# Optimization experiments

Measured on AMD Instinct MI355X. Metric: run time of the kernel, lower is better.

## Reference

```python
import jax, jax.numpy as jnp
import numpy as np

LN_EPS = 1e-5

def _layernorm(x):
    # LayerNorm over last dim, no affine params (elementwise_affine=False)
    mu = jnp.mean(x, axis=-1, keepdims=True)
    var = jnp.var(x, axis=-1, keepdims=True)
    return (x - mu) / jnp.sqrt(var + LN_EPS)

def setup_inputs() -> dict:
    key = jax.random.key(0)
    k1, k2 = jax.random.split(key)
    B, S, D_IN, D_OUT = 4, 2048, 4096, 4096
    x = jax.random.normal(k1, (B, S, D_IN), dtype=jnp.float32)
    # kaiming-uniform-ish init scale (exact distribution irrelevant for correctness baseline)
    bound = 1.0 / np.sqrt(D_IN)
    weight = jax.random.uniform(k2, (D_OUT, D_IN), dtype=jnp.float32, minval=-bound, maxval=bound)
    return {"x": x, "weight": weight}

def reference(x, weight):
    # weight mean-centering and scalar scale beta
    w_centered = weight - jnp.mean(weight)
    beta = jnp.mean(jnp.abs(w_centered))
    x_norm = _layernorm(x)
    w_bin = jnp.sign(w_centered)                       # [D_out, D_in] in {-1,0,+1}
    out = jnp.einsum('bsi,oi->bso', x_norm, w_bin)     # dense GEMM on binarized weights
    return out * beta
```

## Files before the change

kernel.cpp:

```cpp
#include <hip/hip_runtime.h>
#include <hip/hip_bf16.h>
#include <stdint.h>


typedef __bf16 bf16x8 __attribute__((ext_vector_type(8)));
typedef float f32x4 __attribute__((ext_vector_type(4)));

#define LDS_BUF 65536


__device__ __forceinline__ void gl_lds16(const void* g, void* l) {
  __builtin_amdgcn_global_load_lds(
      (const __attribute__((address_space(1))) void*)g,
      (__attribute__((address_space(3))) void*)l,
      16, 0, 0);
}

__device__ __forceinline__ unsigned short f2bf_rne(float f) {
  unsigned int u = __float_as_uint(f);
  unsigned int r = (u + 0x7FFFu + ((u >> 16) & 1u)) >> 16;
  return (unsigned short)r;
}

__device__ __forceinline__ float wave_red(float v) {
#pragma unroll
  for (int o = 32; o > 0; o >>= 1) v += __shfl_down(v, o, 64);
  return v;
}

__device__ __forceinline__ float block_red(float v) {
  __shared__ float tmp[4];
  const int wave = threadIdx.x >> 6, lane = threadIdx.x & 63;
  v = wave_red(v);
  if (lane == 0) tmp[wave] = v;
  __syncthreads();
  float r = 0.f;
  if (threadIdx.x == 0) r = tmp[0] + tmp[1] + tmp[2] + tmp[3];
  return r;
}


__global__ void zero_kernel(float* p) {
  if (threadIdx.x < 8) p[threadIdx.x] = 0.f;
}

__global__ __launch_bounds__(256) void wsum_kernel(const float* __restrict__ w,
                                                   float* __restrict__ scal, int n4) {
  int idx = blockIdx.x * 256 + threadIdx.x;
  int stride = gridDim.x * 256;
  const float4* w4 = (const float4*)w;
  float s = 0.f;
  for (int i = idx; i < n4; i += stride) {
    float4 a = w4[i];
    s += a.x + a.y + a.z + a.w;
  }
  float tot = block_red(s);
  if (threadIdx.x == 0) atomicAdd(&scal[0], tot);
}

__global__ __launch_bounds__(256) void wbin_kernel(const float* __restrict__ w,
                                                   float* __restrict__ scal,
                                                   unsigned short* __restrict__ wb,
                                                   int n4, float inv_n) {
  const float mean = scal[0] * inv_n;
  int idx = blockIdx.x * 256 + threadIdx.x;
  int stride = gridDim.x * 256;
  const float4* w4 = (const float4*)w;
  ushort4* wb4 = (ushort4*)wb;
  float sa = 0.f;
  for (int i = idx; i < n4; i += stride) {
    float4 a = w4[i];
    float dx = a.x - mean, dy = a.y - mean, dz = a.z - mean, dw = a.w - mean;
    sa += fabsf(dx) + fabsf(dy) + fabsf(dz) + fabsf(dw);
    ushort4 o;
    o.x = dx > 0.f ? 0x3F80u : (dx < 0.f ? 0xBF80u : 0u);
    o.y = dy > 0.f ? 0x3F80u : (dy < 0.f ? 0xBF80u : 0u);
    o.z = dz > 0.f ? 0x3F80u : (dz < 0.f ? 0xBF80u : 0u);
    o.w = dw > 0.f ? 0x3F80u : (dw < 0.f ? 0xBF80u : 0u);
    wb4[i] = o;
  }
  float tot = block_red(sa);
  if (threadIdx.x == 0) atomicAdd(&scal[1], tot);
}

__global__ __launch_bounds__(256) void ln_kernel(const float* __restrict__ x,
                                                 __bf16* __restrict__ xn) {
  const int row = blockIdx.x;
  const float4* xr = (const float4*)(x + (size_t)row * 4096);
  const int tid = threadIdx.x;
  float4 v[4];
  float s = 0.f, ss = 0.f;
#pragma unroll
  for (int t = 0; t < 4; t++) {
    float4 a = xr[t * 256 + tid];
    v[t] = a;
    s += a.x + a.y + a.z + a.w;
    ss += a.x * a.x + a.y * a.y + a.z * a.z + a.w * a.w;
  }
#pragma unroll
  for (int o = 32; o > 0; o >>= 1) {
    s += __shfl_down(s, o, 64);
    ss += __shfl_down(ss, o, 64);
  }
  __shared__ float rs[8];
  const int wave = tid >> 6, lane = tid & 63;
  if (lane == 0) { rs[wave] = s; rs[4 + wave] = ss; }
  __syncthreads();
  s = rs[0] + rs[1] + rs[2] + rs[3];
  ss = rs[4] + rs[5] + rs[6] + rs[7];
  const float mu = s * (1.0f / 4096.0f);
  const float var = ss * (1.0f / 4096.0f) - mu * mu;
  const float rstd = rsqrtf(var + 1e-5f);
  ushort4* xw = (ushort4*)((unsigned short*)xn + (size_t)row * 4096);
#pragma unroll
  for (int t = 0; t < 4; t++) {
    float4 a = v[t];
    ushort4 o;
    o.x = f2bf_rne((a.x - mu) * rstd);
    o.y = f2bf_rne((a.y - mu) * rstd);
    o.z = f2bf_rne((a.z - mu) * rstd);
    o.w = f2bf_rne((a.w - mu) * rstd);
    xw[t * 256 + tid] = o;
  }
}


__global__ __launch_bounds__(512, 2) void gemm_kernel(
    const __bf16* __restrict__ A, const __bf16* __restrict__ Bm,
    float* __restrict__ C, const float* __restrict__ scal,
    float beta_scale, int M, int N, int K) {
  extern __shared__ __align__(16) char sm[];

  const int tid = threadIdx.x;
  const int wave = tid >> 6, lane = tid & 63;
  const int wm = wave >> 2, wn = wave & 3;
  const int fr = lane & 15, hi4 = lane >> 4;

  const int nwg = gridDim.x;
  const int swz = (blockIdx.x & 7) * (nwg >> 3) + (blockIdx.x >> 3);
  const int TM = M >> 8;
  const int tm = swz % TM, tn = swz / TM;
  const int rowBase = tm << 8, colBase = tn << 8;

  const int s = (tid & 7) ^ ((tid >> 3) & 7);
  const int rb = ((tid >> 2) & ~1) | (s >> 2);
  const int colOff = (s & 3) << 3;
  const __bf16* srcA0 = A + (size_t)(rowBase + (rb & 63) + ((rb >> 6) << 7)) * K + colOff;
  const __bf16* srcB0 = Bm + (size_t)(colBase + rb) * K + colOff;
  const int waveOff = wave << 10;

  int abase = (wm << 12) + (fr << 6) + (hi4 << 4);
  abase ^= ((abase >> 7) & 7) << 4;
  int bbase = ((wn >> 1) << 13) + ((wn & 1) << 12) + (fr << 6) + (hi4 << 4);
  bbase ^= ((bbase >> 7) & 7) << 4;

  char* const buf0 = sm;
  char* const buf1 = sm + LDS_BUF;

  auto stA = [&](char* buf, int k, int qm, int kt) {
    gl_lds16(srcA0 + (size_t)(qm << 6) * K + (kt + (k << 5)),
             buf + (k << 14) + (qm << 13) + waveOff);
  };
  auto stB = [&](char* buf, int k, int half, int kt) {
    gl_lds16(srcB0 + (size_t)(half << 7) * K + (kt + (k << 5)),
             buf + 32768 + (k << 14) + (half << 13) + waveOff);
  };

  f32x4 acc[8][4];
#pragma unroll
  for (int i = 0; i < 8; i++)
#pragma unroll
    for (int j = 0; j < 4; j++) acc[i][j] = (f32x4){0.f, 0.f, 0.f, 0.f};

  const int NT = K >> 6;

  stA(buf0, 0, 0, 0); stA(buf0, 0, 1, 0); stB(buf0, 0, 0, 0); stB(buf0, 0, 1, 0);
  stA(buf0, 1, 0, 0); stA(buf0, 1, 1, 0); stB(buf0, 1, 0, 0); stB(buf0, 1, 1, 0);
  stA(buf1, 0, 0, 64); stA(buf1, 0, 1, 64); stB(buf1, 0, 0, 64);
  stA(buf1, 1, 0, 64); stB(buf1, 0, 1, 64);
  asm volatile("s_waitcnt vmcnt(5)" ::: "memory");
  asm volatile("s_barrier" ::: "memory");

  for (int T = 0; T < NT; ++T) {
    char* const bc = (T & 1) ? buf1 : buf0;
    char* const bo = (T & 1) ? buf0 : buf1;
    const int kt1 = ((T + 1 < NT) ? T + 1 : NT - 1) << 6;
    const int kt2 = ((T + 2 < NT) ? T + 2 : NT - 1) << 6;

    bf16x8 a0[4], a1[4], b0[4], b1[4];

#pragma unroll
    for (int i = 0; i < 4; i++) a0[i] = *(const bf16x8*)(bc + abase + (i << 10));
#pragma unroll
    for (int j = 0; j < 4; j++) b0[j] = *(const bf16x8*)(bc + 32768 + bbase + (j << 10));
    stA(bo, 1, 1, kt1); stB(bo, 1, 0, kt1); stB(bo, 1, 1, kt1);
    asm volatile("s_barrier" ::: "memory");
    asm volatile("s_waitcnt lgkmcnt(0)" ::: "memory");
    __builtin_amdgcn_s_setprio(1);
#pragma unroll
    for (int i = 0; i < 4; i++)
#pragma unroll
      for (int j = 0; j < 4; j++)
        acc[i][j] = __builtin_amdgcn_mfma_f32_16x16x32_bf16(a0[i], b0[j], acc[i][j], 0, 0, 0);
    __builtin_amdgcn_s_setprio(0);
#pragma unroll
    for (int i = 0; i < 4; i++) a1[i] = *(const bf16x8*)(bc + (1 << 13) + abase + (i << 10));
    asm volatile("s_barrier" ::: "memory");

    stA(bc, 0, 0, kt2);
    asm volatile("s_barrier" ::: "memory");
    asm volatile("s_waitcnt lgkmcnt(0)" ::: "memory");
    __builtin_amdgcn_s_setprio(1);
#pragma unroll
    for (int i = 0; i < 4; i++)
#pragma unroll
      for (int j = 0; j < 4; j++)
        acc[4 + i][j] = __builtin_amdgcn_mfma_f32_16x16x32_bf16(a1[i], b0[j], acc[4 + i][j], 0, 0, 0);
    __builtin_amdgcn_s_setprio(0);
#pragma unroll
    for (int i = 0; i < 4; i++) a0[i] = *(const bf16x8*)(bc + (1 << 14) + abase + (i << 10));
#pragma unroll
    for (int j = 0; j < 4; j++) b1[j] = *(const bf16x8*)(bc + 32768 + (1 << 14) + bbase + (j << 10));
    asm volatile("s_barrier" ::: "memory");

    stA(bc, 0, 1, kt2); stB(bc, 0, 0, kt2);
    asm volatile("s_barrier" ::: "memory");
    asm volatile("s_waitcnt lgkmcnt(0)" ::: "memory");
    __builtin_amdgcn_s_setprio(1);
#pragma unroll
    for (int i = 0; i < 4; i++)
#pragma unroll
      for (int j = 0; j < 4; j++)
        acc[i][j] = __builtin_amdgcn_mfma_f32_16x16x32_bf16(a0[i], b1[j], acc[i][j], 0, 0, 0);
    __builtin_amdgcn_s_setprio(0);
#pragma unroll
    for (int i = 0; i < 4; i++) a1[i] = *(const bf16x8*)(bc + (1 << 14) + (1 << 13) + abase + (i << 10));
    asm volatile("s_barrier" ::: "memory");

    stA(bc, 1, 0, kt2); stB(bc, 0, 1, kt2);
    asm volatile("s_waitcnt vmcnt(5)" ::: "memory");
    asm volatile("s_barrier" ::: "memory");
    asm volatile("s_waitcnt lgkmcnt(0)" ::: "memory");
    __builtin_amdgcn_s_setprio(1);
#pragma unroll
    for (int i = 0; i < 4; i++)
#pragma unroll
      for (int j = 0; j < 4; j++)
        acc[4 + i][j] = __builtin_amdgcn_mfma_f32_16x16x32_bf16(a1[i], b1[j], acc[4 + i][j], 0, 0, 0);
    __builtin_amdgcn_s_setprio(0);
    asm volatile("s_barrier" ::: "memory");
  }

  asm volatile("s_waitcnt vmcnt(0)" ::: "memory");

  const float beta = scal[1] * beta_scale;
  const int orow0 = rowBase + (wm << 7) + (hi4 << 2);
  const int ocol = colBase + (wn << 6) + fr;
#pragma unroll
  for (int mf = 0; mf < 8; mf++)
#pragma unroll
    for (int j = 0; j < 4; j++)
#pragma unroll
      for (int r = 0; r < 4; r++)
        C[(size_t)(orow0 + mf * 16 + r) * N + (ocol + j * 16)] = acc[mf][j][r] * beta;
}


extern "C" void kernel_launch(void* const* d_in, const int* in_sizes, int n_in,
                              void* d_out, int out_size, void* d_ws, size_t ws_size,
                              hipStream_t stream) {
  const float* x = (const float*)d_in[0];
  const float* w = (const float*)d_in[1];
  float* out = (float*)d_out;

  const int K = 4096;
  const int M = in_sizes[0] / K;
  const int N = in_sizes[1] / K;
  const int nw = N * K;
  const float inv_nw = 1.0f / (float)nw;

  char* ws = (char*)d_ws;
  float* scal = (float*)ws;
  __bf16* wbin = (__bf16*)(ws + 256);
  __bf16* xn = (__bf16*)(ws + 256 + (size_t)nw * 2);

  static int attr_done = 0;
  if (!attr_done) {
    hipFuncSetAttribute((const void*)gemm_kernel,
                        hipFuncAttributeMaxDynamicSharedMemorySize, 2 * LDS_BUF);
    attr_done = 1;
  }

  zero_kernel<<<1, 64, 0, stream>>>(scal);
  wsum_kernel<<<1024, 256, 0, stream>>>(w, scal, nw / 4);
  wbin_kernel<<<1024, 256, 0, stream>>>(w, scal, (unsigned short*)wbin, nw / 4, inv_nw);
  ln_kernel<<<M, 256, 0, stream>>>(x, xn);
  const int nwg = (M >> 8) * (N >> 8);
  gemm_kernel<<<dim3(nwg), 512, 2 * LDS_BUF, stream>>>(xn, wbin, out, scal, inv_nw, M, N, K);
}
```

Measured before the change: 570.9 us.

## Software-pipeline LDS fragment loads ahead of MFMA groups and unroll by two

Moves each LDS fragment read so it is issued before the MFMA block that precedes its use, including prefetching the next tile's first fragments at the end of the current tile. sched_group_barrier hints then place the LDS reads alongside the MFMAs. The K loop is unrolled by two so the buffer pointers become compile-time constants. The aim is to hide LDS read latency behind matrix math, at the cost of more live vector registers and reliance on the compiler honoring the scheduling hints. The final prefetch reads buffer bo after the last tile, which is harmless but is an extra read.

Result: slower. 587.9 us (+3.0%).

```diff
diff --git a/kernel.cpp b/kernel.cpp
--- a/kernel.cpp
+++ b/kernel.cpp
@@ -7,6 +7,12 @@
 typedef float f32x4 __attribute__((ext_vector_type(4)));
 
 #define LDS_BUF 65536
+
+#define MFMA16(AA, BB, OFF)                                                   \
+  _Pragma("unroll") for (int i = 0; i < 4; i++)                               \
+  _Pragma("unroll") for (int j = 0; j < 4; j++)                               \
+      acc[(OFF) + i][j] = __builtin_amdgcn_mfma_f32_16x16x32_bf16(            \
+          AA[i], BB[j], acc[(OFF) + i][j], 0, 0, 0);
 
 
 __device__ __forceinline__ void gl_lds16(const void* g, void* l) {
@@ -172,6 +178,8 @@
 #pragma unroll
     for (int j = 0; j < 4; j++) acc[i][j] = (f32x4){0.f, 0.f, 0.f, 0.f};
 
+  bf16x8 a0[4], a1[4], b0[4], b1[4];
+
   const int NT = K >> 6;
 
   stA(buf0, 0, 0, 0); stA(buf0, 0, 1, 0); stB(buf0, 0, 0, 0); stB(buf0, 0, 1, 0);
@@ -180,75 +188,72 @@
   stA(buf1, 1, 0, 64); stB(buf1, 0, 1, 64);
   asm volatile("s_waitcnt vmcnt(5)" ::: "memory");
   asm volatile("s_barrier" ::: "memory");
-
-  for (int T = 0; T < NT; ++T) {
-    char* const bc = (T & 1) ? buf1 : buf0;
-    char* const bo = (T & 1) ? buf0 : buf1;
+#pragma unroll
+  for (int i = 0; i < 4; i++) a0[i] = *(const bf16x8*)(buf0 + abase + (i << 10));
+#pragma unroll
+  for (int j = 0; j < 4; j++) b0[j] = *(const bf16x8*)(buf0 + 32768 + bbase + (j << 10));
+
+  auto tile = [&](char* const bc, char* const bo, int T) {
     const int kt1 = ((T + 1 < NT) ? T + 1 : NT - 1) << 6;
     const int kt2 = ((T + 2 < NT) ? T + 2 : NT - 1) << 6;
 
-    bf16x8 a0[4], a1[4], b0[4], b1[4];
-
-#pragma unroll
-    for (int i = 0; i < 4; i++) a0[i] = *(const bf16x8*)(bc + abase + (i << 10));
-#pragma unroll
-    for (int j = 0; j < 4; j++) b0[j] = *(const bf16x8*)(bc + 32768 + bbase + (j << 10));
     stA(bo, 1, 1, kt1); stB(bo, 1, 0, kt1); stB(bo, 1, 1, kt1);
     asm volatile("s_barrier" ::: "memory");
     asm volatile("s_waitcnt lgkmcnt(0)" ::: "memory");
+#pragma unroll
+    for (int i = 0; i < 4; i++) a1[i] = *(const bf16x8*)(bc + (1 << 13) + abase + (i << 10));
     __builtin_amdgcn_s_setprio(1);
-#pragma unroll
-    for (int i = 0; i < 4; i++)
-#pragma unroll
-      for (int j = 0; j < 4; j++)
-        acc[i][j] = __builtin_amdgcn_mfma_f32_16x16x32_bf16(a0[i], b0[j], acc[i][j], 0, 0, 0);
+    MFMA16(a0, b0, 0)
     __builtin_amdgcn_s_setprio(0);
-#pragma unroll
-    for (int i = 0; i < 4; i++) a1[i] = *(const bf16x8*)(bc + (1 << 13) + abase + (i << 10));
+    __builtin_amdgcn_sched_group_barrier(0x100, 4, 0);
+    __builtin_amdgcn_sched_group_barrier(0x008, 16, 0);
     asm volatile("s_barrier" ::: "memory");
 
     stA(bc, 0, 0, kt2);
     asm volatile("s_barrier" ::: "memory");
     asm volatile("s_waitcnt lgkmcnt(0)" ::: "memory");
+#pragma unroll
+    for (int i = 0; i < 4; i++) a0[i] = *(const bf16x8*)(bc + (1 << 14) + abase + (i << 10));
+#pragma unroll
+    for (int j = 0; j < 4; j++) b1[j] = *(const bf16x8*)(bc + 32768 + (1 << 14) + bbase + (j << 10));
     __builtin_amdgcn_s_setprio(1);
-#pragma unroll
-    for (int i = 0; i < 4; i++)
-#pragma unroll
-      for (int j = 0; j < 4; j++)
-        acc[4 + i][j] = __builtin_amdgcn_mfma_f32_16x16x32_bf16(a1[i], b0[j], acc[4 + i][j], 0, 0, 0);
+    MFMA16(a1, b0, 4)
     __builtin_amdgcn_s_setprio(0);
-#pragma unroll
-    for (int i = 0; i < 4; i++) a0[i] = *(const bf16x8*)(bc + (1 << 14) + abase + (i << 10));
-#pragma unroll
-    for (int j = 0; j < 4; j++) b1[j] = *(const bf16x8*)(bc + 32768 + (1 << 14) + bbase + (j << 10));
+    __builtin_amdgcn_sched_group_barrier(0x100, 8, 0);
+    __builtin_amdgcn_sched_group_barrier(0x008, 16, 0);
     asm volatile("s_barrier" ::: "memory");
 
     stA(bc, 0, 1, kt2); stB(bc, 0, 0, kt2);
     asm volatile("s_barrier" ::: "memory");
     asm volatile("s_waitcnt lgkmcnt(0)" ::: "memory");
+#pragma unroll
+    for (int i = 0; i < 4; i++) a1[i] = *(const bf16x8*)(bc + (1 << 14) + (1 << 13) + abase + (i << 10));
     __builtin_amdgcn_s_setprio(1);
-#pragma unroll
-    for (int i = 0; i < 4; i++)
-#pragma unroll
-      for (int j = 0; j < 4; j++)
-        acc[i][j] = __builtin_amdgcn_mfma_f32_16x16x32_bf16(a0[i], b1[j], acc[i][j], 0, 0, 0);
+    MFMA16(a0, b1, 0)
     __builtin_amdgcn_s_setprio(0);
-#pragma unroll
-    for (int i = 0; i < 4; i++) a1[i] = *(const bf16x8*)(bc + (1 << 14) + (1 << 13) + abase + (i << 10));
+    __builtin_amdgcn_sched_group_barrier(0x100, 4, 0);
+    __builtin_amdgcn_sched_group_barrier(0x008, 16, 0);
     asm volatile("s_barrier" ::: "memory");
 
     stA(bc, 1, 0, kt2); stB(bc, 0, 1, kt2);
     asm volatile("s_waitcnt vmcnt(5)" ::: "memory");
     asm volatile("s_barrier" ::: "memory");
     asm volatile("s_waitcnt lgkmcnt(0)" ::: "memory");
+#pragma unroll
+    for (int i = 0; i < 4; i++) a0[i] = *(const bf16x8*)(bo + abase + (i << 10));
+#pragma unroll
+    for (int j = 0; j < 4; j++) b0[j] = *(const bf16x8*)(bo + 32768 + bbase + (j << 10));
     __builtin_amdgcn_s_setprio(1);
-#pragma unroll
-    for (int i = 0; i < 4; i++)
-#pragma unroll
-      for (int j = 0; j < 4; j++)
-        acc[4 + i][j] = __builtin_amdgcn_mfma_f32_16x16x32_bf16(a1[i], b1[j], acc[4 + i][j], 0, 0, 0);
+    MFMA16(a1, b1, 4)
     __builtin_amdgcn_s_setprio(0);
-    asm volatile("s_barrier" ::: "memory");
+    __builtin_amdgcn_sched_group_barrier(0x100, 8, 0);
+    __builtin_amdgcn_sched_group_barrier(0x008, 16, 0);
+    asm volatile("s_barrier" ::: "memory");
+  };
+
+  for (int T = 0; T < NT; T += 2) {
+    tile(buf0, buf1, T);
+    tile(buf1, buf0, T + 1);
   }
 
   asm volatile("s_waitcnt vmcnt(0)" ::: "memory");
```
